# Performance work log

Hardware: AMD Instinct MI355X
Metric: run time of the kernel (lower is better)

## Reference

```python
import jax, jax.numpy as jnp
import numpy as np

B, LAT, FRAME, HID, E, GH = 4096, 64, 512, 1024, 8, 128
IN1 = LAT + FRAME      # 576, fc1/gate input
IN2 = LAT + HID        # 1088, fc2/fc3 input
OUT = FRAME            # 512, num_future_frames * frame_size


def setup_inputs() -> dict:
    key = jax.random.key(0)
    ks = jax.random.split(key, 16)
    s = lambda fan_in: 1.0 / np.sqrt(fan_in)
    inp = {
        "z": jax.random.normal(ks[0], (B, LAT), jnp.float32),
        "c": jax.random.normal(ks[1], (B, FRAME), jnp.float32),
        # expert-mixed layers: weight [E, in, out], bias [E, out]
        "w0": jax.random.uniform(ks[2], (E, IN1, HID), jnp.float32, -s(IN1), s(IN1)),
        "b0": jax.random.uniform(ks[3], (E, HID), jnp.float32, -s(IN1), s(IN1)),
        "w1": jax.random.uniform(ks[4], (E, IN2, HID), jnp.float32, -s(IN2), s(IN2)),
        "b1": jax.random.uniform(ks[5], (E, HID), jnp.float32, -s(IN2), s(IN2)),
        "w2": jax.random.uniform(ks[6], (E, IN2, OUT), jnp.float32, -s(IN2), s(IN2)),
        "b2": jax.random.uniform(ks[7], (E, OUT), jnp.float32, -s(IN2), s(IN2)),
        # gate MLP
        "gw1": jax.random.uniform(ks[8], (IN1, GH), jnp.float32, -s(IN1), s(IN1)),
        "gb1": jax.random.uniform(ks[9], (GH,), jnp.float32, -s(IN1), s(IN1)),
        "gw2": jax.random.uniform(ks[10], (GH, GH), jnp.float32, -s(GH), s(GH)),
        "gb2": jax.random.uniform(ks[11], (GH,), jnp.float32, -s(GH), s(GH)),
        "gw3": jax.random.uniform(ks[12], (GH, E), jnp.float32, -s(GH), s(GH)),
        "gb3": jax.random.uniform(ks[13], (E,), jnp.float32, -s(GH), s(GH)),
    }
    return inp


def _mixed_layer(coef, x, w, b):
    # per-expert projection then softmax-weighted mix: same math as
    # baddbmm(coef@b, x, (coef@flat(w)).view(B,in,out)) in the original.
    ye = jnp.einsum('bi,eio->beo', x, w)          # [B, E, out]
    return jnp.einsum('be,beo->bo', coef, ye) + coef @ b


def reference(z, c, w0, b0, w1, b1, w2, b2, gw1, gb1, gw2, gb2, gw3, gb3):
    x0 = jnp.concatenate([z, c], axis=1)           # [B, IN1]
    h = jax.nn.elu(x0 @ gw1 + gb1)
    h = jax.nn.elu(h @ gw2 + gb2)
    coef = jax.nn.softmax(h @ gw3 + gb3, axis=1)   # [B, E]

    out = jax.nn.elu(_mixed_layer(coef, x0, w0, b0))
    out = jax.nn.elu(_mixed_layer(coef, jnp.concatenate([z, out], axis=1), w1, b1))
    out = _mixed_layer(coef, jnp.concatenate([z, out], axis=1), w2, b2)
    return out
```

## Files before the change

### kernel.cpp

```cpp
#include <hip/hip_runtime.h>
#include <cstdint>
#include <cstddef>

#define B_    4096
#define LAT   64
#define FRAME 512
#define HID   1024
#define NE    8
#define GH    128
#define IN1   576
#define IN2   1088

typedef _Float16 half8 __attribute__((ext_vector_type(8)));
typedef _Float16 half4 __attribute__((ext_vector_type(4)));
typedef float  f32x4  __attribute__((ext_vector_type(4)));

__device__ inline void async16(const void* g, void* l) {
  __builtin_amdgcn_global_load_lds(
      (__attribute__((address_space(1))) void*)(void*)g,
      (__attribute__((address_space(3))) void*)l, 16, 0, 0);
}

__device__ inline float elu(float v) { return v > 0.f ? v : expm1f(v); }

__global__ __launch_bounds__(256) void prep_weights(
    const float* __restrict__ w0, const float* __restrict__ w1,
    const float* __restrict__ w2, const float* __restrict__ gw1,
    const float* __restrict__ gw2,
    _Float16* __restrict__ Wt0, _Float16* __restrict__ Wt1,
    _Float16* __restrict__ Wt2, _Float16* __restrict__ gw1T,
    _Float16* __restrict__ gw2T)
{
  __shared__ float t[64][65];
  int bid = blockIdx.x;
  const float* in; _Float16* out; int K, N, kt, nt;
  if (bid < 1152) {
    const int e = bid / 144, rem = bid % 144;
    K = IN1; N = HID; kt = rem / 16; nt = rem % 16;
    in = w0 + (size_t)e * K * N; out = Wt0 + (size_t)e * N * K;
  } else if (bid < 3328) {
    const int i = bid - 1152, e = i / 272, rem = i % 272;
    K = IN2; N = HID; kt = rem / 16; nt = rem % 16;
    in = w1 + (size_t)e * K * N; out = Wt1 + (size_t)e * N * K;
  } else if (bid < 4416) {
    const int i = bid - 3328, e = i / 136, rem = i % 136;
    K = IN2; N = FRAME; kt = rem / 8; nt = rem % 8;
    in = w2 + (size_t)e * K * N; out = Wt2 + (size_t)e * N * K;
  } else if (bid < 4434) {
    const int i = bid - 4416;
    K = IN1; N = GH; kt = i / 2; nt = i % 2;
    in = gw1; out = gw1T;
  } else {
    const int i = bid - 4434;
    K = GH; N = GH; kt = i / 2; nt = i % 2;
    in = gw2; out = gw2T;
  }
  const int k0 = kt * 64, n0 = nt * 64;
  const int lr = threadIdx.x >> 4;
  const int lc = (threadIdx.x & 15) * 4;
  #pragma unroll
  for (int rr = 0; rr < 4; ++rr) {
    const int k = rr * 16 + lr;
    f32x4 v = *(const f32x4*)(in + (size_t)(k0 + k) * N + n0 + lc);
    t[k][lc] = v[0]; t[k][lc + 1] = v[1]; t[k][lc + 2] = v[2]; t[k][lc + 3] = v[3];
  }
  __syncthreads();
  #pragma unroll
  for (int rr = 0; rr < 4; ++rr) {
    const int n = rr * 16 + lr;
    half4 o;
    #pragma unroll
    for (int q = 0; q < 4; ++q) o[q] = (_Float16)t[lc + q][n];
    *(half4*)(out + (size_t)(n0 + n) * K + k0 + lc) = o;
  }
}

__global__ __launch_bounds__(256) void gate_mfma(
    const float* __restrict__ z, const float* __restrict__ c,
    const _Float16* __restrict__ gw1T,
    const _Float16* __restrict__ gw2T,
    const float* __restrict__ gb1, const float* __restrict__ gb2,
    const float* __restrict__ gw3, const float* __restrict__ gb3,
    float* __restrict__ coef)
{
  __shared__ _Float16 h_lds[64][136];
  __shared__ float    h2_lds[64][129];
  __shared__ float    gw3s[128 * 8];
  const int tid = threadIdx.x;
  const int wave = tid >> 6, lane = tid & 63;
  const int quad = lane >> 4, l16 = lane & 15;
  const int r0 = blockIdx.x * 64;

  for (int i = tid; i < 128 * 8; i += 256) gw3s[i] = gw3[i];

  f32x4 acc[8];
  #pragma unroll
  for (int nt = 0; nt < 8; ++nt)
    #pragma unroll
    for (int r = 0; r < 4; ++r) acc[nt][r] = 0.f;

  #pragma unroll 2
  for (int s = 0; s < 18; ++s) {
    const int k0 = s * 32;
    half8 af;
    {
      const size_t row = r0 + wave * 16 + l16;
      const float* src = (k0 < LAT) ? z + row * LAT + k0 + quad * 8
                                    : c + row * FRAME + (k0 - LAT) + quad * 8;
      f32x4 lo = *(const f32x4*)src, hi = *(const f32x4*)(src + 4);
      #pragma unroll
      for (int j = 0; j < 4; ++j) { af[j] = (_Float16)lo[j]; af[j + 4] = (_Float16)hi[j]; }
    }
    half8 bfr[8];
    #pragma unroll
    for (int nt = 0; nt < 8; ++nt)
      bfr[nt] = *(const half8*)(gw1T + (size_t)(nt * 16 + l16) * 576 + k0 + quad * 8);
    #pragma unroll
    for (int nt = 0; nt < 8; ++nt)
      acc[nt] = __builtin_amdgcn_mfma_f32_16x16x32_f16(af, bfr[nt], acc[nt], 0, 0, 0);
  }
  #pragma unroll
  for (int nt = 0; nt < 8; ++nt)
    #pragma unroll
    for (int r = 0; r < 4; ++r) {
      const int rowl = wave * 16 + quad * 4 + r;
      const int col = nt * 16 + l16;
      h_lds[rowl][col] = (_Float16)elu(acc[nt][r] + gb1[col]);
    }
  __syncthreads();

  f32x4 acc2[8];
  #pragma unroll
  for (int nt = 0; nt < 8; ++nt)
    #pragma unroll
    for (int r = 0; r < 4; ++r) acc2[nt][r] = 0.f;
  #pragma unroll
  for (int s = 0; s < 4; ++s) {
    const int k0 = s * 32;
    half8 af = *(const half8*)&h_lds[wave * 16 + l16][k0 + quad * 8];
    half8 bfr[8];
    #pragma unroll
    for (int nt = 0; nt < 8; ++nt)
      bfr[nt] = *(const half8*)(gw2T + (size_t)(nt * 16 + l16) * 128 + k0 + quad * 8);
    #pragma unroll
    for (int nt = 0; nt < 8; ++nt)
      acc2[nt] = __builtin_amdgcn_mfma_f32_16x16x32_f16(af, bfr[nt], acc2[nt], 0, 0, 0);
  }
  #pragma unroll
  for (int nt = 0; nt < 8; ++nt)
    #pragma unroll
    for (int r = 0; r < 4; ++r) {
      const int rowl = wave * 16 + quad * 4 + r;
      const int col = nt * 16 + l16;
      h2_lds[rowl][col] = elu(acc2[nt][r] + gb2[col]);
    }
  __syncthreads();

  {
    const int row = tid >> 2, q = tid & 3;
    float l2v[2] = { gb3[2 * q], gb3[2 * q + 1] };
    for (int k = 0; k < 128; ++k) {
      const float hv = h2_lds[row][k];
      l2v[0] += hv * gw3s[k * 8 + 2 * q];
      l2v[1] += hv * gw3s[k * 8 + 2 * q + 1];
    }
    float m = fmaxf(l2v[0], l2v[1]);
    m = fmaxf(m, __shfl_xor(m, 1));
    m = fmaxf(m, __shfl_xor(m, 2));
    float e0 = expf(l2v[0] - m), e1 = expf(l2v[1] - m);
    float s = e0 + e1;
    s += __shfl_xor(s, 1);
    s += __shfl_xor(s, 2);
    const float inv = 1.f / s;
    float2 o = { e0 * inv, e1 * inv };
    *(float2*)&coef[(size_t)(r0 + row) * NE + 2 * q] = o;
  }
}

__global__ __launch_bounds__(256) void build_x1(
    const float* __restrict__ z, const float* __restrict__ c,
    _Float16* __restrict__ x1)
{
  const int idx4 = blockIdx.x * 256 + threadIdx.x;
  const int b = idx4 / (IN1 / 4), j = (idx4 - b * (IN1 / 4)) * 4;
  f32x4 v = (j < LAT) ? *(const f32x4*)(z + (size_t)b * LAT + j)
                      : *(const f32x4*)(c + (size_t)b * FRAME + (j - LAT));
  half4 o;
  #pragma unroll
  for (int q = 0; q < 4; ++q) o[q] = (_Float16)v[q];
  *(half4*)(x1 + (size_t)b * IN1 + j) = o;
}

template<int KDIM, int NOUT, int EG>
__global__ __launch_bounds__(256, 2) void gemm_moe(
    const _Float16* __restrict__ X,
    const _Float16* __restrict__ Wt,
    const float* __restrict__ coef,
    const float* __restrict__ bias,
    float* __restrict__ part)
{
  __shared__ __align__(16) _Float16 As[128 * 64];
  __shared__ __align__(16) _Float16 Bs[2][128 * 64];
  __shared__ float coefS[128 * EG];
  __shared__ float biasS[EG * 128];

  const int tid = threadIdx.x;
  const int wave = tid >> 6, lane = tid & 63;
  const int wm = wave & 1, wn = wave >> 1;
  const int quad = lane >> 4, l16 = lane & 15;
  const int bm0 = blockIdx.x * 128, bn0 = blockIdx.y * 128;
  const int ebase = blockIdx.z * EG;

  for (int i = tid; i < 128 * EG; i += 256)
    coefS[i] = coef[(size_t)(bm0 + i / EG) * NE + ebase + (i % EG)];
  for (int i = tid; i < EG * 128; i += 256)
    biasS[i] = bias[(size_t)(ebase + (i >> 7)) * NOUT + bn0 + (i & 127)];
  __syncthreads();

  _Float16 ch[4][EG];
  #pragma unroll
  for (int mi = 0; mi < 4; ++mi)
    #pragma unroll
    for (int e = 0; e < EG; ++e)
      ch[mi][e] = (_Float16)coefS[(wm * 64 + mi * 16 + l16) * EG + e];

  f32x4 acc[4][4];
  #pragma unroll
  for (int mi = 0; mi < 4; ++mi)
    #pragma unroll
    for (int ni = 0; ni < 4; ++ni)
      #pragma unroll
      for (int r = 0; r < 4; ++r) acc[mi][ni][r] = 0.f;

  const int srow  = wave * 8 + (lane >> 3);
  const int skoff = (((lane & 7) ^ ((lane >> 3) & 7)) * 8);

  constexpr int K0S = KDIM / 64;
  for (int k0i = 0; k0i < K0S; ++k0i) {
    const int k0 = k0i * 64;
    #pragma unroll
    for (int it = 0; it < 4; ++it)
      async16(X + (size_t)(bm0 + it * 32 + srow) * KDIM + k0 + skoff,
              &As[it * 2048 + wave * 512]);
    {
      const size_t eoff = (size_t)ebase * NOUT * KDIM;
      #pragma unroll
      for (int it = 0; it < 4; ++it)
        async16(Wt + eoff + (size_t)(bn0 + it * 32 + srow) * KDIM + k0 + skoff,
                &Bs[0][it * 2048 + wave * 512]);
    }
    __syncthreads();

    half8 af[2][4];
    #pragma unroll
    for (int ks = 0; ks < 2; ++ks)
      #pragma unroll
      for (int mi = 0; mi < 4; ++mi) {
        const int r = wm * 64 + mi * 16 + l16;
        const int g = (ks * 4 + quad) ^ (r & 7);
        af[ks][mi] = *(const half8*)&As[r * 64 + g * 8];
      }

    #pragma unroll
    for (int eo = 0; eo < EG; ++eo) {
      if (eo + 1 < EG) {
        const size_t eoff = (size_t)(ebase + eo + 1) * NOUT * KDIM;
        #pragma unroll
        for (int it = 0; it < 4; ++it)
          async16(Wt + eoff + (size_t)(bn0 + it * 32 + srow) * KDIM + k0 + skoff,
                  &Bs[(eo + 1) & 1][it * 2048 + wave * 512]);
      }
      const _Float16* bsrc = Bs[eo & 1];
      #pragma unroll
      for (int ks = 0; ks < 2; ++ks) {
        half8 bv[4];
        #pragma unroll
        for (int ni = 0; ni < 4; ++ni) {
          const int r = wn * 64 + ni * 16 + l16;
          const int g = (ks * 4 + quad) ^ (r & 7);
          bv[ni] = *(const half8*)&bsrc[r * 64 + g * 8];
        }
        #pragma unroll
        for (int mi = 0; mi < 4; ++mi) {
          const half8 afs = af[ks][mi] * ch[mi][eo];
          #pragma unroll
          for (int ni = 0; ni < 4; ++ni)
            acc[mi][ni] = __builtin_amdgcn_mfma_f32_16x16x32_f16(
                afs, bv[ni], acc[mi][ni], 0, 0, 0);
        }
      }
      __syncthreads();
    }
  }

  float* po = part + (size_t)blockIdx.z * B_ * NOUT;
  #pragma unroll
  for (int mi = 0; mi < 4; ++mi)
    #pragma unroll
    for (int r = 0; r < 4; ++r) {
      const int m_loc = wm * 64 + mi * 16 + quad * 4 + r;
      #pragma unroll
      for (int ni = 0; ni < 4; ++ni) {
        const int n_loc = wn * 64 + ni * 16 + l16;
        float v = acc[mi][ni][r];
        #pragma unroll
        for (int e = 0; e < EG; ++e)
          v += coefS[m_loc * EG + e] * biasS[e * 128 + n_loc];
        po[(size_t)(bm0 + m_loc) * NOUT + bn0 + n_loc] = v;
      }
    }
}

__global__ __launch_bounds__(256) void expand_x(
    const float* __restrict__ part,
    const float* __restrict__ z,
    _Float16* __restrict__ xn)
{
  const int idx4 = blockIdx.x * 256 + threadIdx.x;
  const int b = idx4 / (IN2 / 4), j = (idx4 - b * (IN2 / 4)) * 4;
  half4 o;
  if (j < LAT) {
    f32x4 v = *(const f32x4*)(z + (size_t)b * LAT + j);
    #pragma unroll
    for (int q = 0; q < 4; ++q) o[q] = (_Float16)v[q];
  } else {
    const int h = j - LAT;
    f32x4 v0 = *(const f32x4*)(part + (size_t)b * HID + h);
    f32x4 v1 = *(const f32x4*)(part + (size_t)B_ * HID + (size_t)b * HID + h);
    #pragma unroll
    for (int q = 0; q < 4; ++q) o[q] = (_Float16)elu(v0[q] + v1[q]);
  }
  *(half4*)(xn + (size_t)b * IN2 + j) = o;
}

__global__ __launch_bounds__(256) void final_out(
    const float* __restrict__ part,
    float* __restrict__ out)
{
  const int idx4 = (blockIdx.x * 256 + threadIdx.x) * 4;
  f32x4 v = *(const f32x4*)(part + idx4);
  #pragma unroll
  for (int s = 1; s < 4; ++s) {
    f32x4 p = *(const f32x4*)(part + (size_t)s * B_ * FRAME + idx4);
    #pragma unroll
    for (int q = 0; q < 4; ++q) v[q] += p[q];
  }
  *(f32x4*)(out + idx4) = v;
}


extern "C" void kernel_launch(void* const* d_in, const int* in_sizes, int n_in,
                              void* d_out, int out_size, void* d_ws, size_t ws_size,
                              hipStream_t stream)
{
  const float* z   = (const float*)d_in[0];
  const float* c   = (const float*)d_in[1];
  const float* w0  = (const float*)d_in[2];
  const float* b0  = (const float*)d_in[3];
  const float* w1  = (const float*)d_in[4];
  const float* b1  = (const float*)d_in[5];
  const float* w2  = (const float*)d_in[6];
  const float* b2  = (const float*)d_in[7];
  const float* gw1 = (const float*)d_in[8];
  const float* gb1 = (const float*)d_in[9];
  const float* gw2 = (const float*)d_in[10];
  const float* gb2 = (const float*)d_in[11];
  const float* gw3 = (const float*)d_in[12];
  const float* gb3 = (const float*)d_in[13];
  float* out = (float*)d_out;
  char* ws = (char*)d_ws;

  float*    coef = (float*)    (ws + 0);
  _Float16* x1   = (_Float16*) (ws + 131072);
  _Float16* x2   = (_Float16*) (ws + 4849664);
  _Float16* x3   = (_Float16*) (ws + 13762560);
  _Float16* Wt0  = (_Float16*) (ws + 22675456);
  _Float16* Wt1  = (_Float16*) (ws + 32112640);
  _Float16* Wt2  = (_Float16*) (ws + 49938432);
  float*    part = (float*)    (ws + 58851328);
  _Float16* gw1T = (_Float16*) (ws + 92405760);
  _Float16* gw2T = (_Float16*) (ws + 92553216);

  prep_weights<<<4438, 256, 0, stream>>>(w0, w1, w2, gw1, gw2,
                                         Wt0, Wt1, Wt2, gw1T, gw2T);
  gate_mfma<<<64, 256, 0, stream>>>(z, c, gw1T, gw2T, gb1, gb2, gw3, gb3, coef);
  build_x1<<<(B_ * IN1 / 4) / 256, 256, 0, stream>>>(z, c, x1);

  gemm_moe<IN1, HID, 4><<<dim3(32, 8, 2), 256, 0, stream>>>(x1, Wt0, coef, b0, part);
  expand_x<<<(B_ * IN2 / 4) / 256, 256, 0, stream>>>(part, z, x2);

  gemm_moe<IN2, HID, 4><<<dim3(32, 8, 2), 256, 0, stream>>>(x2, Wt1, coef, b1, part);
  expand_x<<<(B_ * IN2 / 4) / 256, 256, 0, stream>>>(part, z, x3);

  gemm_moe<IN2, FRAME, 2><<<dim3(32, 4, 4), 256, 0, stream>>>(x3, Wt2, coef, b2, part);
  final_out<<<(B_ * FRAME / 4) / 256, 256, 0, stream>>>(part, out);
}
```

Baseline: 341.9 us.

## Use taller 256-row tiles with more expert splits for first two MoE GEMMs

Adds a gemm_tall kernel that stages 256 rows of X per block (8 MFMA row tiles per wave) to reuse each weight tile across more rows, and splits experts into 4 groups of 2 instead of 2 groups of 4. expand_x is templated on the number of partial sums so it can reduce 4 partials. Workspace layout is reshuffled so x1 and x2 share a buffer, making room for a larger partial buffer. The trade-off is more accumulator registers per thread (128 floats), which may limit occupancy or spill, and double the partial-sum traffic through global memory.

Measured after the change: 733.4 us. 2.15x slower.

```diff
diff --git a/kernel.cpp b/kernel.cpp
--- a/kernel.cpp
+++ b/kernel.cpp
@@ -192,6 +192,126 @@
 }
 
 template<int KDIM, int NOUT, int EG>
+__global__ __launch_bounds__(256, 2) void gemm_tall(
+    const _Float16* __restrict__ X,
+    const _Float16* __restrict__ Wt,
+    const float* __restrict__ coef,
+    const float* __restrict__ bias,
+    float* __restrict__ part)
+{
+  __shared__ __align__(16) _Float16 As[256 * 64];
+  __shared__ __align__(16) _Float16 Bs[2][128 * 64];
+  __shared__ float coefS[256 * EG];
+  __shared__ float biasS[EG * 128];
+
+  const int tid = threadIdx.x;
+  const int wave = tid >> 6, lane = tid & 63;
+  const int wm = wave & 1, wn = wave >> 1;
+  const int quad = lane >> 4, l16 = lane & 15;
+  const int bm0 = blockIdx.x * 256, bn0 = blockIdx.y * 128;
+  const int ebase = blockIdx.z * EG;
+
+  for (int i = tid; i < 256 * EG; i += 256)
+    coefS[i] = coef[(size_t)(bm0 + i / EG) * NE + ebase + (i % EG)];
+  for (int i = tid; i < EG * 128; i += 256)
+    biasS[i] = bias[(size_t)(ebase + (i >> 7)) * NOUT + bn0 + (i & 127)];
+  __syncthreads();
+
+  _Float16 ch[8][EG];
+  #pragma unroll
+  for (int mi = 0; mi < 8; ++mi)
+    #pragma unroll
+    for (int e = 0; e < EG; ++e)
+      ch[mi][e] = (_Float16)coefS[(wm * 128 + mi * 16 + l16) * EG + e];
+
+  f32x4 acc[8][4];
+  #pragma unroll
+  for (int mi = 0; mi < 8; ++mi)
+    #pragma unroll
+    for (int ni = 0; ni < 4; ++ni)
+      #pragma unroll
+      for (int r = 0; r < 4; ++r) acc[mi][ni][r] = 0.f;
+
+  const int srow  = wave * 8 + (lane >> 3);
+  const int skoff = (((lane & 7) ^ ((lane >> 3) & 7)) * 8);
+
+  constexpr int K0S = KDIM / 64;
+  for (int k0i = 0; k0i < K0S; ++k0i) {
+    const int k0 = k0i * 64;
+    #pragma unroll
+    for (int it = 0; it < 8; ++it)
+      async16(X + (size_t)(bm0 + it * 32 + srow) * KDIM + k0 + skoff,
+              &As[it * 2048 + wave * 512]);
+    {
+      const size_t eoff = (size_t)ebase * NOUT * KDIM;
+      #pragma unroll
+      for (int it = 0; it < 4; ++it)
+        async16(Wt + eoff + (size_t)(bn0 + it * 32 + srow) * KDIM + k0 + skoff,
+                &Bs[0][it * 2048 + wave * 512]);
+    }
+    __syncthreads();
+
+    half8 af[2][8];
+    #pragma unroll
+    for (int ks = 0; ks < 2; ++ks)
+      #pragma unroll
+      for (int mi = 0; mi < 8; ++mi) {
+        const int r = wm * 128 + mi * 16 + l16;
+        const int g = (ks * 4 + quad) ^ (r & 7);
+        af[ks][mi] = *(const half8*)&As[r * 64 + g * 8];
+      }
+
+    #pragma unroll
+    for (int eo = 0; eo < EG; ++eo) {
+      if (eo + 1 < EG) {
+        const size_t eoff = (size_t)(ebase + eo + 1) * NOUT * KDIM;
+        #pragma unroll
+        for (int it = 0; it < 4; ++it)
+          async16(Wt + eoff + (size_t)(bn0 + it * 32 + srow) * KDIM + k0 + skoff,
+                  &Bs[(eo + 1) & 1][it * 2048 + wave * 512]);
+      }
+      const _Float16* bsrc = Bs[eo & 1];
+      #pragma unroll
+      for (int ks = 0; ks < 2; ++ks) {
+        half8 bv[4];
+        #pragma unroll
+        for (int ni = 0; ni < 4; ++ni) {
+          const int r = wn * 64 + ni * 16 + l16;
+          const int g = (ks * 4 + quad) ^ (r & 7);
+          bv[ni] = *(const half8*)&bsrc[r * 64 + g * 8];
+        }
+        #pragma unroll
+        for (int mi = 0; mi < 8; ++mi) {
+          const half8 afs = af[ks][mi] * ch[mi][eo];
+          #pragma unroll
+          for (int ni = 0; ni < 4; ++ni)
+            acc[mi][ni] = __builtin_amdgcn_mfma_f32_16x16x32_f16(
+                afs, bv[ni], acc[mi][ni], 0, 0, 0);
+        }
+      }
+      __syncthreads();
+    }
+  }
+
+  float* po = part + (size_t)blockIdx.z * B_ * NOUT;
+  #pragma unroll
+  for (int mi = 0; mi < 8; ++mi)
+    #pragma unroll
+    for (int r = 0; r < 4; ++r) {
+      const int m_loc = wm * 128 + mi * 16 + quad * 4 + r;
+      #pragma unroll
+      for (int ni = 0; ni < 4; ++ni) {
+        const int n_loc = wn * 64 + ni * 16 + l16;
+        float v = acc[mi][ni][r];
+        #pragma unroll
+        for (int e = 0; e < EG; ++e)
+          v += coefS[m_loc * EG + e] * biasS[e * 128 + n_loc];
+        po[(size_t)(bm0 + m_loc) * NOUT + bn0 + n_loc] = v;
+      }
+    }
+}
+
+template<int KDIM, int NOUT, int EG>
 __global__ __launch_bounds__(256, 2) void gemm_moe(
     const _Float16* __restrict__ X,
     const _Float16* __restrict__ Wt,
@@ -311,6 +431,7 @@
     }
 }
 
+template<int NS>
 __global__ __launch_bounds__(256) void expand_x(
     const float* __restrict__ part,
     const float* __restrict__ z,
@@ -325,10 +446,15 @@
     for (int q = 0; q < 4; ++q) o[q] = (_Float16)v[q];
   } else {
     const int h = j - LAT;
-    f32x4 v0 = *(const f32x4*)(part + (size_t)b * HID + h);
-    f32x4 v1 = *(const f32x4*)(part + (size_t)B_ * HID + (size_t)b * HID + h);
-    #pragma unroll
-    for (int q = 0; q < 4; ++q) o[q] = (_Float16)elu(v0[q] + v1[q]);
+    f32x4 v = *(const f32x4*)(part + (size_t)b * HID + h);
+    #pragma unroll
+    for (int s = 1; s < NS; ++s) {
+      f32x4 p = *(const f32x4*)(part + (size_t)s * B_ * HID + (size_t)b * HID + h);
+      #pragma unroll
+      for (int q = 0; q < 4; ++q) v[q] += p[q];
+    }
+    #pragma unroll
+    for (int q = 0; q < 4; ++q) o[q] = (_Float16)elu(v[q]);
   }
   *(half4*)(xn + (size_t)b * IN2 + j) = o;
 }
@@ -371,26 +497,26 @@
   char* ws = (char*)d_ws;
 
   float*    coef = (float*)    (ws + 0);
+  _Float16* x2   = (_Float16*) (ws + 131072);
   _Float16* x1   = (_Float16*) (ws + 131072);
-  _Float16* x2   = (_Float16*) (ws + 4849664);
-  _Float16* x3   = (_Float16*) (ws + 13762560);
-  _Float16* Wt0  = (_Float16*) (ws + 22675456);
-  _Float16* Wt1  = (_Float16*) (ws + 32112640);
-  _Float16* Wt2  = (_Float16*) (ws + 49938432);
-  float*    part = (float*)    (ws + 58851328);
-  _Float16* gw1T = (_Float16*) (ws + 92405760);
-  _Float16* gw2T = (_Float16*) (ws + 92553216);
+  _Float16* x3   = (_Float16*) (ws + 9043968);
+  _Float16* Wt1  = (_Float16*) (ws + 17956864);
+  _Float16* Wt2  = (_Float16*) (ws + 35782656);
+  float*    part = (float*)    (ws + 44695552);
+  _Float16* Wt0  = (_Float16*) (ws + 111804416);
+  _Float16* gw1T = (_Float16*) (ws + 121241600);
+  _Float16* gw2T = (_Float16*) (ws + 121389056);
 
   prep_weights<<<4438, 256, 0, stream>>>(w0, w1, w2, gw1, gw2,
                                          Wt0, Wt1, Wt2, gw1T, gw2T);
   gate_mfma<<<64, 256, 0, stream>>>(z, c, gw1T, gw2T, gb1, gb2, gw3, gb3, coef);
   build_x1<<<(B_ * IN1 / 4) / 256, 256, 0, stream>>>(z, c, x1);
 
-  gemm_moe<IN1, HID, 4><<<dim3(32, 8, 2), 256, 0, stream>>>(x1, Wt0, coef, b0, part);
-  expand_x<<<(B_ * IN2 / 4) / 256, 256, 0, stream>>>(part, z, x2);
-
-  gemm_moe<IN2, HID, 4><<<dim3(32, 8, 2), 256, 0, stream>>>(x2, Wt1, coef, b1, part);
-  expand_x<<<(B_ * IN2 / 4) / 256, 256, 0, stream>>>(part, z, x3);
+  gemm_tall<IN1, HID, 2><<<dim3(16, 8, 4), 256, 0, stream>>>(x1, Wt0, coef, b0, part);
+  expand_x<4><<<(B_ * IN2 / 4) / 256, 256, 0, stream>>>(part, z, x2);
+
+  gemm_tall<IN2, HID, 2><<<dim3(16, 8, 4), 256, 0, stream>>>(x2, Wt1, coef, b1, part);
+  expand_x<4><<<(B_ * IN2 / 4) / 256, 256, 0, stream>>>(part, z, x3);
 
   gemm_moe<IN2, FRAME, 2><<<dim3(32, 4, 4), 256, 0, stream>>>(x3, Wt2, coef, b2, part);
   final_out<<<(B_ * FRAME / 4) / 256, 256, 0, stream>>>(part, out);
```

## Fuse expert split-K into single GEMM with ELU epilogue, drop partial buffers

Applied to the files above, without the earlier changes.

Each GEMM now loops over all 8 experts inside one block instead of splitting experts across blockIdx.z. This removes the fp32 partial-sum buffer and the separate expand/final reduction kernels, and ELU plus fp16 conversion happen in the GEMM epilogue, which writes directly into the next layer's input. Weight tiles are loaded straight from global memory into registers rather than staged through LDS, and the A tile is double-buffered in LDS. Tiles are smaller (128x64 or 64x64) so there are still enough blocks. The trade-off is less weight reuse per block and global-latency-bound B loads.

Result: slower. 509.7 us (+49.1%).

```diff
diff --git a/kernel.cpp b/kernel.cpp
--- a/kernel.cpp
+++ b/kernel.cpp
@@ -177,9 +177,10 @@
   }
 }
 
-__global__ __launch_bounds__(256) void build_x1(
+__global__ __launch_bounds__(256) void build_x(
     const float* __restrict__ z, const float* __restrict__ c,
-    _Float16* __restrict__ x1)
+    _Float16* __restrict__ x1, _Float16* __restrict__ x2,
+    _Float16* __restrict__ x3)
 {
   const int idx4 = blockIdx.x * 256 + threadIdx.x;
   const int b = idx4 / (IN1 / 4), j = (idx4 - b * (IN1 / 4)) * 4;
@@ -189,163 +190,132 @@
   #pragma unroll
   for (int q = 0; q < 4; ++q) o[q] = (_Float16)v[q];
   *(half4*)(x1 + (size_t)b * IN1 + j) = o;
-}
-
-template<int KDIM, int NOUT, int EG>
-__global__ __launch_bounds__(256, 2) void gemm_moe(
+  if (j < LAT) {
+    *(half4*)(x2 + (size_t)b * IN2 + j) = o;
+    *(half4*)(x3 + (size_t)b * IN2 + j) = o;
+  }
+}
+
+template<int KDIM, int NOUT, int MI, int NI, bool F16OUT>
+__global__ __launch_bounds__(256, 2) void gemm_fused(
     const _Float16* __restrict__ X,
     const _Float16* __restrict__ Wt,
     const float* __restrict__ coef,
     const float* __restrict__ bias,
-    float* __restrict__ part)
-{
-  __shared__ __align__(16) _Float16 As[128 * 64];
-  __shared__ __align__(16) _Float16 Bs[2][128 * 64];
-  __shared__ float coefS[128 * EG];
-  __shared__ float biasS[EG * 128];
+    _Float16* __restrict__ xn,
+    float* __restrict__ outf)
+{
+  constexpr int M = 32 * MI, N = 32 * NI;
+  __shared__ __align__(16) _Float16 As[2][M * 64];
+  __shared__ float coefS[M * NE];
+  __shared__ float biasS[NE * N];
 
   const int tid = threadIdx.x;
   const int wave = tid >> 6, lane = tid & 63;
   const int wm = wave & 1, wn = wave >> 1;
   const int quad = lane >> 4, l16 = lane & 15;
-  const int bm0 = blockIdx.x * 128, bn0 = blockIdx.y * 128;
-  const int ebase = blockIdx.z * EG;
-
-  for (int i = tid; i < 128 * EG; i += 256)
-    coefS[i] = coef[(size_t)(bm0 + i / EG) * NE + ebase + (i % EG)];
-  for (int i = tid; i < EG * 128; i += 256)
-    biasS[i] = bias[(size_t)(ebase + (i >> 7)) * NOUT + bn0 + (i & 127)];
-  __syncthreads();
-
-  _Float16 ch[4][EG];
-  #pragma unroll
-  for (int mi = 0; mi < 4; ++mi)
-    #pragma unroll
-    for (int e = 0; e < EG; ++e)
-      ch[mi][e] = (_Float16)coefS[(wm * 64 + mi * 16 + l16) * EG + e];
-
-  f32x4 acc[4][4];
-  #pragma unroll
-  for (int mi = 0; mi < 4; ++mi)
-    #pragma unroll
-    for (int ni = 0; ni < 4; ++ni)
-      #pragma unroll
-      for (int r = 0; r < 4; ++r) acc[mi][ni][r] = 0.f;
+  const int bm0 = blockIdx.x * M, bn0 = blockIdx.y * N;
+
+  for (int i = tid; i < M * NE; i += 256)
+    coefS[i] = coef[(size_t)(bm0 + (i >> 3)) * NE + (i & 7)];
+  for (int i = tid; i < NE * N; i += 256)
+    biasS[i] = bias[(size_t)(i / N) * NOUT + bn0 + (i % N)];
 
   const int srow  = wave * 8 + (lane >> 3);
   const int skoff = (((lane & 7) ^ ((lane >> 3) & 7)) * 8);
 
+  int rowoff[NI];
+  #pragma unroll
+  for (int ni = 0; ni < NI; ++ni)
+    rowoff[ni] = (bn0 + wn * 16 * NI + ni * 16 + l16) * KDIM;
+  const int koffB = quad * 8;
+
+  #define STAGE_A(k0v, buf) \
+    { _Pragma("unroll") \
+      for (int it = 0; it < MI; ++it) \
+        async16(X + (size_t)(bm0 + it * 32 + srow) * KDIM + (k0v) + skoff, \
+                &(buf)[it * 2048 + wave * 512]); }
+
+  half8 bv[2][2 * NI];
+  auto loadB = [&](int e, int k0v, half8* dst) {
+    const _Float16* p = Wt + (size_t)e * NOUT * KDIM + k0v + koffB;
+    #pragma unroll
+    for (int ks = 0; ks < 2; ++ks)
+      #pragma unroll
+      for (int ni = 0; ni < NI; ++ni)
+        dst[ks * NI + ni] = *(const half8*)(p + rowoff[ni] + ks * 32);
+  };
+
+  STAGE_A(0, As[0]);
+  loadB(0, 0, bv[0]);
+  __syncthreads();
+
+  _Float16 ch[MI][NE];
+  #pragma unroll
+  for (int mi = 0; mi < MI; ++mi)
+    #pragma unroll
+    for (int e = 0; e < NE; ++e)
+      ch[mi][e] = (_Float16)coefS[(wm * 16 * MI + mi * 16 + l16) * NE + e];
+
+  f32x4 acc[MI][NI];
+  #pragma unroll
+  for (int mi = 0; mi < MI; ++mi)
+    #pragma unroll
+    for (int ni = 0; ni < NI; ++ni)
+      #pragma unroll
+      for (int r = 0; r < 4; ++r) acc[mi][ni][r] = 0.f;
+
   constexpr int K0S = KDIM / 64;
   for (int k0i = 0; k0i < K0S; ++k0i) {
-    const int k0 = k0i * 64;
-    #pragma unroll
-    for (int it = 0; it < 4; ++it)
-      async16(X + (size_t)(bm0 + it * 32 + srow) * KDIM + k0 + skoff,
-              &As[it * 2048 + wave * 512]);
-    {
-      const size_t eoff = (size_t)ebase * NOUT * KDIM;
-      #pragma unroll
-      for (int it = 0; it < 4; ++it)
-        async16(Wt + eoff + (size_t)(bn0 + it * 32 + srow) * KDIM + k0 + skoff,
-                &Bs[0][it * 2048 + wave * 512]);
-    }
-    __syncthreads();
-
-    half8 af[2][4];
+    const int k0 = k0i * 64, ap = k0i & 1;
+    half8 af[2][MI];
     #pragma unroll
     for (int ks = 0; ks < 2; ++ks)
       #pragma unroll
-      for (int mi = 0; mi < 4; ++mi) {
-        const int r = wm * 64 + mi * 16 + l16;
+      for (int mi = 0; mi < MI; ++mi) {
+        const int r = wm * 16 * MI + mi * 16 + l16;
         const int g = (ks * 4 + quad) ^ (r & 7);
-        af[ks][mi] = *(const half8*)&As[r * 64 + g * 8];
+        af[ks][mi] = *(const half8*)&As[ap][r * 64 + g * 8];
       }
-
-    #pragma unroll
-    for (int eo = 0; eo < EG; ++eo) {
-      if (eo + 1 < EG) {
-        const size_t eoff = (size_t)(ebase + eo + 1) * NOUT * KDIM;
+    if (k0i + 1 < K0S) STAGE_A(k0 + 64, As[1 - ap]);
+
+    #pragma unroll
+    for (int eo = 0; eo < NE; ++eo) {
+      if (eo + 1 < NE)           loadB(eo + 1, k0, bv[(eo + 1) & 1]);
+      else if (k0i + 1 < K0S)    loadB(0, k0 + 64, bv[0]);
+      const half8* bq = bv[eo & 1];
+      #pragma unroll
+      for (int ks = 0; ks < 2; ++ks)
         #pragma unroll
-        for (int it = 0; it < 4; ++it)
-          async16(Wt + eoff + (size_t)(bn0 + it * 32 + srow) * KDIM + k0 + skoff,
-                  &Bs[(eo + 1) & 1][it * 2048 + wave * 512]);
-      }
-      const _Float16* bsrc = Bs[eo & 1];
-      #pragma unroll
-      for (int ks = 0; ks < 2; ++ks) {
-        half8 bv[4];
-        #pragma unroll
-        for (int ni = 0; ni < 4; ++ni) {
-          const int r = wn * 64 + ni * 16 + l16;
-          const int g = (ks * 4 + quad) ^ (r & 7);
-          bv[ni] = *(const half8*)&bsrc[r * 64 + g * 8];
-        }
-        #pragma unroll
-        for (int mi = 0; mi < 4; ++mi) {
+        for (int mi = 0; mi < MI; ++mi) {
           const half8 afs = af[ks][mi] * ch[mi][eo];
           #pragma unroll
-          for (int ni = 0; ni < 4; ++ni)
+          for (int ni = 0; ni < NI; ++ni)
             acc[mi][ni] = __builtin_amdgcn_mfma_f32_16x16x32_f16(
-                afs, bv[ni], acc[mi][ni], 0, 0, 0);
+                afs, bq[ks * NI + ni], acc[mi][ni], 0, 0, 0);
         }
-      }
-      __syncthreads();
-    }
-  }
-
-  float* po = part + (size_t)blockIdx.z * B_ * NOUT;
-  #pragma unroll
-  for (int mi = 0; mi < 4; ++mi)
+    }
+    __syncthreads();
+  }
+  #undef STAGE_A
+
+  #pragma unroll
+  for (int mi = 0; mi < MI; ++mi)
     #pragma unroll
     for (int r = 0; r < 4; ++r) {
-      const int m_loc = wm * 64 + mi * 16 + quad * 4 + r;
-      #pragma unroll
-      for (int ni = 0; ni < 4; ++ni) {
-        const int n_loc = wn * 64 + ni * 16 + l16;
+      const int m_loc = wm * 16 * MI + mi * 16 + quad * 4 + r;
+      const size_t grow = (size_t)(bm0 + m_loc);
+      #pragma unroll
+      for (int ni = 0; ni < NI; ++ni) {
+        const int n_loc = wn * 16 * NI + ni * 16 + l16;
         float v = acc[mi][ni][r];
         #pragma unroll
-        for (int e = 0; e < EG; ++e)
-          v += coefS[m_loc * EG + e] * biasS[e * 128 + n_loc];
-        po[(size_t)(bm0 + m_loc) * NOUT + bn0 + n_loc] = v;
+        for (int e = 0; e < NE; ++e)
+          v += coefS[m_loc * NE + e] * biasS[e * N + n_loc];
+        if (F16OUT) xn[grow * IN2 + LAT + bn0 + n_loc] = (_Float16)elu(v);
+        else        outf[grow * NOUT + bn0 + n_loc] = v;
       }
     }
-}
-
-__global__ __launch_bounds__(256) void expand_x(
-    const float* __restrict__ part,
-    const float* __restrict__ z,
-    _Float16* __restrict__ xn)
-{
-  const int idx4 = blockIdx.x * 256 + threadIdx.x;
-  const int b = idx4 / (IN2 / 4), j = (idx4 - b * (IN2 / 4)) * 4;
-  half4 o;
-  if (j < LAT) {
-    f32x4 v = *(const f32x4*)(z + (size_t)b * LAT + j);
-    #pragma unroll
-    for (int q = 0; q < 4; ++q) o[q] = (_Float16)v[q];
-  } else {
-    const int h = j - LAT;
-    f32x4 v0 = *(const f32x4*)(part + (size_t)b * HID + h);
-    f32x4 v1 = *(const f32x4*)(part + (size_t)B_ * HID + (size_t)b * HID + h);
-    #pragma unroll
-    for (int q = 0; q < 4; ++q) o[q] = (_Float16)elu(v0[q] + v1[q]);
-  }
-  *(half4*)(xn + (size_t)b * IN2 + j) = o;
-}
-
-__global__ __launch_bounds__(256) void final_out(
-    const float* __restrict__ part,
-    float* __restrict__ out)
-{
-  const int idx4 = (blockIdx.x * 256 + threadIdx.x) * 4;
-  f32x4 v = *(const f32x4*)(part + idx4);
-  #pragma unroll
-  for (int s = 1; s < 4; ++s) {
-    f32x4 p = *(const f32x4*)(part + (size_t)s * B_ * FRAME + idx4);
-    #pragma unroll
-    for (int q = 0; q < 4; ++q) v[q] += p[q];
-  }
-  *(f32x4*)(out + idx4) = v;
 }
 
 
@@ -377,21 +347,18 @@
   _Float16* Wt0  = (_Float16*) (ws + 22675456);
   _Float16* Wt1  = (_Float16*) (ws + 32112640);
   _Float16* Wt2  = (_Float16*) (ws + 49938432);
-  float*    part = (float*)    (ws + 58851328);
-  _Float16* gw1T = (_Float16*) (ws + 92405760);
-  _Float16* gw2T = (_Float16*) (ws + 92553216);
+  _Float16* gw1T = (_Float16*) (ws + 58851328);
+  _Float16* gw2T = (_Float16*) (ws + 58998784);
 
   prep_weights<<<4438, 256, 0, stream>>>(w0, w1, w2, gw1, gw2,
                                          Wt0, Wt1, Wt2, gw1T, gw2T);
   gate_mfma<<<64, 256, 0, stream>>>(z, c, gw1T, gw2T, gb1, gb2, gw3, gb3, coef);
-  build_x1<<<(B_ * IN1 / 4) / 256, 256, 0, stream>>>(z, c, x1);
-
-  gemm_moe<IN1, HID, 4><<<dim3(32, 8, 2), 256, 0, stream>>>(x1, Wt0, coef, b0, part);
-  expand_x<<<(B_ * IN2 / 4) / 256, 256, 0, stream>>>(part, z, x2);
-
-  gemm_moe<IN2, HID, 4><<<dim3(32, 8, 2), 256, 0, stream>>>(x2, Wt1, coef, b1, part);
-  expand_x<<<(B_ * IN2 / 4) / 256, 256, 0, stream>>>(part, z, x3);
-
-  gemm_moe<IN2, FRAME, 2><<<dim3(32, 4, 4), 256, 0, stream>>>(x3, Wt2, coef, b2, part);
-  final_out<<<(B_ * FRAME / 4) / 256, 256, 0, stream>>>(part, out);
-}
+  build_x<<<(B_ * IN1 / 4) / 256, 256, 0, stream>>>(z, c, x1, x2, x3);
+
+  gemm_fused<IN1, HID, 4, 2, true><<<dim3(32, 16), 256, 0, stream>>>(
+      x1, Wt0, coef, b0, x2, nullptr);
+  gemm_fused<IN2, HID, 4, 2, true><<<dim3(32, 16), 256, 0, stream>>>(
+      x2, Wt1, coef, b1, x3, nullptr);
+  gemm_fused<IN2, FRAME, 2, 2, false><<<dim3(64, 8), 256, 0, stream>>>(
+      x3, Wt2, coef, b2, nullptr, out);
+}
```

## Fuse expert loop and ELU epilogue into single GEMM, drop split-expert partials

Applied to the files above, without the earlier changes.

Adds a gemm_fused kernel for the first two mixed layers. It loops over all 8 experts inside one block, scaling the A fragment by the per-row fp16 coefficient and double-buffering the expert weight tiles. The kernel applies bias and ELU and writes fp16 activations straight into the next layer's input buffer. This removes the fp32 partial buffers and the two expand_x kernels, and build_x now writes the z prefix into x2 and x3. In exchange, the N tile is smaller (64), there is a sync per expert step, and multiplying activations by coef in fp16 may cost some precision.

Result: slower. 366.3 us (+7.1%).

```diff
diff --git a/kernel.cpp b/kernel.cpp
--- a/kernel.cpp
+++ b/kernel.cpp
@@ -177,9 +177,10 @@
   }
 }
 
-__global__ __launch_bounds__(256) void build_x1(
+__global__ __launch_bounds__(256) void build_x(
     const float* __restrict__ z, const float* __restrict__ c,
-    _Float16* __restrict__ x1)
+    _Float16* __restrict__ x1, _Float16* __restrict__ x2,
+    _Float16* __restrict__ x3)
 {
   const int idx4 = blockIdx.x * 256 + threadIdx.x;
   const int b = idx4 / (IN1 / 4), j = (idx4 - b * (IN1 / 4)) * 4;
@@ -189,6 +190,126 @@
   #pragma unroll
   for (int q = 0; q < 4; ++q) o[q] = (_Float16)v[q];
   *(half4*)(x1 + (size_t)b * IN1 + j) = o;
+  if (j < LAT) {
+    *(half4*)(x2 + (size_t)b * IN2 + j) = o;
+    *(half4*)(x3 + (size_t)b * IN2 + j) = o;
+  }
+}
+
+template<int KDIM, int NOUT>
+__global__ __launch_bounds__(256, 2) void gemm_fused(
+    const _Float16* __restrict__ X,
+    const _Float16* __restrict__ Wt,
+    const float* __restrict__ coef,
+    const float* __restrict__ bias,
+    _Float16* __restrict__ xn)
+{
+  __shared__ __align__(16) _Float16 As[128 * 64];
+  __shared__ __align__(16) _Float16 Bs[2][64 * 64];
+  __shared__ float coefS[128 * NE];
+  __shared__ float biasS[NE * 64];
+
+  const int tid = threadIdx.x;
+  const int wave = tid >> 6, lane = tid & 63;
+  const int wm = wave & 1, wn = wave >> 1;
+  const int quad = lane >> 4, l16 = lane & 15;
+  const int bm0 = blockIdx.x * 128, bn0 = blockIdx.y * 64;
+
+  for (int i = tid; i < 128 * NE; i += 256)
+    coefS[i] = coef[(size_t)(bm0 + (i >> 3)) * NE + (i & 7)];
+  for (int i = tid; i < NE * 64; i += 256)
+    biasS[i] = bias[(size_t)(i >> 6) * NOUT + bn0 + (i & 63)];
+  __syncthreads();
+
+  _Float16 ch[4][NE];
+  #pragma unroll
+  for (int mi = 0; mi < 4; ++mi)
+    #pragma unroll
+    for (int e = 0; e < NE; ++e)
+      ch[mi][e] = (_Float16)coefS[(wm * 64 + mi * 16 + l16) * NE + e];
+
+  f32x4 acc[4][2];
+  #pragma unroll
+  for (int mi = 0; mi < 4; ++mi)
+    #pragma unroll
+    for (int ni = 0; ni < 2; ++ni)
+      #pragma unroll
+      for (int r = 0; r < 4; ++r) acc[mi][ni][r] = 0.f;
+
+  const int srow  = wave * 8 + (lane >> 3);
+  const int skoff = (((lane & 7) ^ ((lane >> 3) & 7)) * 8);
+
+  constexpr int K0S = KDIM / 64;
+  for (int k0i = 0; k0i < K0S; ++k0i) {
+    const int k0 = k0i * 64;
+    #pragma unroll
+    for (int it = 0; it < 4; ++it)
+      async16(X + (size_t)(bm0 + it * 32 + srow) * KDIM + k0 + skoff,
+              &As[it * 2048 + wave * 512]);
+    #pragma unroll
+    for (int it = 0; it < 2; ++it)
+      async16(Wt + (size_t)(bn0 + it * 32 + srow) * KDIM + k0 + skoff,
+              &Bs[0][it * 2048 + wave * 512]);
+    __syncthreads();
+
+    half8 af[2][4];
+    #pragma unroll
+    for (int ks = 0; ks < 2; ++ks)
+      #pragma unroll
+      for (int mi = 0; mi < 4; ++mi) {
+        const int r = wm * 64 + mi * 16 + l16;
+        const int g = (ks * 4 + quad) ^ (r & 7);
+        af[ks][mi] = *(const half8*)&As[r * 64 + g * 8];
+      }
+
+    #pragma unroll
+    for (int eo = 0; eo < NE; ++eo) {
+      if (eo + 1 < NE) {
+        const size_t eoff = (size_t)(eo + 1) * NOUT * KDIM;
+        #pragma unroll
+        for (int it = 0; it < 2; ++it)
+          async16(Wt + eoff + (size_t)(bn0 + it * 32 + srow) * KDIM + k0 + skoff,
+                  &Bs[(eo + 1) & 1][it * 2048 + wave * 512]);
+      }
+      const _Float16* bsrc = Bs[eo & 1];
+      #pragma unroll
+      for (int ks = 0; ks < 2; ++ks) {
+        half8 bv[2];
+        #pragma unroll
+        for (int ni = 0; ni < 2; ++ni) {
+          const int r = wn * 32 + ni * 16 + l16;
+          const int g = (ks * 4 + quad) ^ (r & 7);
+          bv[ni] = *(const half8*)&bsrc[r * 64 + g * 8];
+        }
+        #pragma unroll
+        for (int mi = 0; mi < 4; ++mi) {
+          const half8 afs = af[ks][mi] * ch[mi][eo];
+          #pragma unroll
+          for (int ni = 0; ni < 2; ++ni)
+            acc[mi][ni] = __builtin_amdgcn_mfma_f32_16x16x32_f16(
+                afs, bv[ni], acc[mi][ni], 0, 0, 0);
+        }
+      }
+      __syncthreads();
+    }
+  }
+
+  #pragma unroll
+  for (int mi = 0; mi < 4; ++mi)
+    #pragma unroll
+    for (int r = 0; r < 4; ++r) {
+      const int m_loc = wm * 64 + mi * 16 + quad * 4 + r;
+      const size_t grow = (size_t)(bm0 + m_loc);
+      #pragma unroll
+      for (int ni = 0; ni < 2; ++ni) {
+        const int n_loc = wn * 32 + ni * 16 + l16;
+        float v = acc[mi][ni][r];
+        #pragma unroll
+        for (int e = 0; e < NE; ++e)
+          v += coefS[m_loc * NE + e] * biasS[e * 64 + n_loc];
+        xn[grow * IN2 + LAT + bn0 + n_loc] = (_Float16)elu(v);
+      }
+    }
 }
 
 template<int KDIM, int NOUT, int EG>
@@ -309,28 +430,6 @@
         po[(size_t)(bm0 + m_loc) * NOUT + bn0 + n_loc] = v;
       }
     }
-}
-
-__global__ __launch_bounds__(256) void expand_x(
-    const float* __restrict__ part,
-    const float* __restrict__ z,
-    _Float16* __restrict__ xn)
-{
-  const int idx4 = blockIdx.x * 256 + threadIdx.x;
-  const int b = idx4 / (IN2 / 4), j = (idx4 - b * (IN2 / 4)) * 4;
-  half4 o;
-  if (j < LAT) {
-    f32x4 v = *(const f32x4*)(z + (size_t)b * LAT + j);
-    #pragma unroll
-    for (int q = 0; q < 4; ++q) o[q] = (_Float16)v[q];
-  } else {
-    const int h = j - LAT;
-    f32x4 v0 = *(const f32x4*)(part + (size_t)b * HID + h);
-    f32x4 v1 = *(const f32x4*)(part + (size_t)B_ * HID + (size_t)b * HID + h);
-    #pragma unroll
-    for (int q = 0; q < 4; ++q) o[q] = (_Float16)elu(v0[q] + v1[q]);
-  }
-  *(half4*)(xn + (size_t)b * IN2 + j) = o;
 }
 
 __global__ __launch_bounds__(256) void final_out(
@@ -384,14 +483,10 @@
   prep_weights<<<4438, 256, 0, stream>>>(w0, w1, w2, gw1, gw2,
                                          Wt0, Wt1, Wt2, gw1T, gw2T);
   gate_mfma<<<64, 256, 0, stream>>>(z, c, gw1T, gw2T, gb1, gb2, gw3, gb3, coef);
-  build_x1<<<(B_ * IN1 / 4) / 256, 256, 0, stream>>>(z, c, x1);
-
-  gemm_moe<IN1, HID, 4><<<dim3(32, 8, 2), 256, 0, stream>>>(x1, Wt0, coef, b0, part);
-  expand_x<<<(B_ * IN2 / 4) / 256, 256, 0, stream>>>(part, z, x2);
-
-  gemm_moe<IN2, HID, 4><<<dim3(32, 8, 2), 256, 0, stream>>>(x2, Wt1, coef, b1, part);
-  expand_x<<<(B_ * IN2 / 4) / 256, 256, 0, stream>>>(part, z, x3);
-
+  build_x<<<(B_ * IN1 / 4) / 256, 256, 0, stream>>>(z, c, x1, x2, x3);
+
+  gemm_fused<IN1, HID><<<dim3(32, 16), 256, 0, stream>>>(x1, Wt0, coef, b0, x2);
+  gemm_fused<IN2, HID><<<dim3(32, 16), 256, 0, stream>>>(x2, Wt1, coef, b1, x3);
   gemm_moe<IN2, FRAME, 2><<<dim3(32, 4, 4), 256, 0, stream>>>(x3, Wt2, coef, b2, part);
   final_out<<<(B_ * FRAME / 4) / 256, 256, 0, stream>>>(part, out);
 }
```
